# Kernel tuning notes

Measured on AMD Instinct MI355X. Metric: run time of the kernel, lower is better.

Reference implementation:

```python
import jax, jax.numpy as jnp
import numpy as np
from jax import lax

HEADS = 4
SR = 4
LN_EPS = 1e-5


def setup_inputs() -> dict:
    key = jax.random.key(0)
    ks = jax.random.split(key, 8)
    B, N, C = 8, 4096, 256
    w_scale = 0.05  # keep attention logits in a sane range
    return {
        "x": jax.random.normal(ks[0], (B, N, C), jnp.float32),
        "h": 64,
        "w": 64,
        "Wq": jax.random.normal(ks[1], (C, C), jnp.float32) * w_scale,
        "Wkv": jax.random.normal(ks[2], (C, 2 * C), jnp.float32) * w_scale,
        "sr_w": jax.random.normal(ks[3], (C, C, SR, SR), jnp.float32) * w_scale,
        "sr_b": jnp.zeros((C,), jnp.float32),
        "ln_g": jnp.ones((C,), jnp.float32),
        "ln_b": jnp.zeros((C,), jnp.float32),
        "Wo": jax.random.normal(ks[4], (C, C), jnp.float32) * w_scale,
        "bo": jnp.zeros((C,), jnp.float32),
    }


def _layernorm(x, g, b):
    mu = x.mean(-1, keepdims=True)
    var = ((x - mu) ** 2).mean(-1, keepdims=True)
    return (x - mu) * lax.rsqrt(var + LN_EPS) * g + b


def reference(x, h, w, Wq, Wkv, sr_w, sr_b, ln_g, ln_b, Wo, bo):
    B, N, C = x.shape
    hd = C // HEADS
    scale = hd ** -0.5
    # Q projection -> [B, H, N, hd]
    q = (x @ Wq).reshape(B, N, HEADS, hd).transpose(0, 2, 1, 3)
    # spatial reduction of K/V tokens: strided conv + LayerNorm
    x_kv = x.transpose(0, 2, 1).reshape(B, C, h, w)  # b (h w) c -> b c h w
    x_kv = lax.conv_general_dilated(
        x_kv, sr_w, window_strides=(SR, SR), padding="VALID",
        dimension_numbers=("NCHW", "OIHW", "NCHW"))
    x_kv = x_kv + sr_b[None, :, None, None]
    Nk = (h // SR) * (w // SR)
    x_kv = x_kv.reshape(B, C, Nk).transpose(0, 2, 1)  # b c h w -> b (h w) c
    x_kv = _layernorm(x_kv, ln_g, ln_b)
    # KV projection -> k, v each [B, H, Nk, hd]
    kv = (x_kv @ Wkv).reshape(B, Nk, 2, HEADS, hd)
    k = kv[:, :, 0].transpose(0, 2, 1, 3)
    v = kv[:, :, 1].transpose(0, 2, 1, 3)
    # attention: full [B, H, N, Nk] score matrix, softmax over kv axis
    att = jax.nn.softmax(jnp.einsum("bhxd,bhyd->bhxy", q, k) * scale, axis=-1)
    out = jnp.einsum("bhxy,bhyd->bhxd", att, v)
    out = out.transpose(0, 2, 1, 3).reshape(B, N, C)  # b h l d -> b l (h d)
    return out @ Wo + bo
```

## Files before the change

kernel.cpp:

```cpp
#include <hip/hip_runtime.h>

typedef __bf16 bf16;
typedef bf16 bf16x8 __attribute__((ext_vector_type(8)));
typedef bf16 bf16x4 __attribute__((ext_vector_type(4)));
typedef float f32x4 __attribute__((ext_vector_type(4)));

#define MFMA16(a, b, c) __builtin_amdgcn_mfma_f32_16x16x32_bf16(a, b, c, 0, 0, 0)

__device__ __forceinline__ void gload_lds16(const bf16* g, bf16* l) {
  __builtin_amdgcn_global_load_lds(
      (const __attribute__((address_space(1))) void*)g,
      (__attribute__((address_space(3))) void*)l, 16, 0, 0);
}

__global__ void k_prep(const float* __restrict__ x, const float* __restrict__ Wq,
                       const float* __restrict__ Wkv, const float* __restrict__ Wo,
                       const float* __restrict__ srw,
                       bf16* __restrict__ x_bf, bf16* __restrict__ WqT,
                       bf16* __restrict__ WkvT, bf16* __restrict__ WoT,
                       bf16* __restrict__ srwT) {
  int bid = blockIdx.x, tid = threadIdx.x;
  if (bid < 4096) {
    int i = (bid * 256 + tid) * 8;
    float4 v0 = *(const float4*)(x + i);
    float4 v1 = *(const float4*)(x + i + 4);
    bf16x8 o;
    o[0] = (bf16)v0.x; o[1] = (bf16)v0.y; o[2] = (bf16)v0.z; o[3] = (bf16)v0.w;
    o[4] = (bf16)v1.x; o[5] = (bf16)v1.y; o[6] = (bf16)v1.z; o[7] = (bf16)v1.w;
    *(bf16x8*)(x_bf + i) = o;
  } else if (bid < 5120) {
    int id = (bid - 4096) * 256 + tid;
    if (id < 65536) {
      int c = id >> 8, r = id & 255;
      WqT[c * 256 + (r ^ ((c & 7) << 3))] = (bf16)Wq[r * 256 + c];
    } else if (id < 196608) {
      int l = id - 65536;
      int c = l >> 8, r = l & 255;
      WkvT[l] = (bf16)Wkv[r * 512 + c];
    } else {
      int l = id - 196608;
      int c = l >> 8, r = l & 255;
      WoT[l] = (bf16)Wo[r * 256 + c];
    }
  } else {
    int id4 = ((bid - 5120) * 256 + tid) * 4;
    int o = id4 >> 12, rem = id4 & 4095;
    int i = rem >> 4, p = rem & 15;
    float4 v = *(const float4*)(srw + id4);
    srwT[(o << 12) + ((p + 0) << 8) + i] = (bf16)v.x;
    srwT[(o << 12) + ((p + 1) << 8) + i] = (bf16)v.y;
    srwT[(o << 12) + ((p + 2) << 8) + i] = (bf16)v.z;
    srwT[(o << 12) + ((p + 3) << 8) + i] = (bf16)v.w;
  }
}

template <int AMODE, int EMODE>
__global__ __launch_bounds__(256, 2) void k_gemm(
    const bf16* __restrict__ A, const bf16* __restrict__ Bt,
    void* __restrict__ Cout, const float* __restrict__ bias,
    int M, int N, int K) {
  constexpr int LDT = 72;
  __shared__ alignas(16) bf16 As[64 * LDT];
  __shared__ alignas(16) bf16 Bs[64 * LDT];
  int tid = threadIdx.x;
  int m0 = blockIdx.x * 64, n0 = blockIdx.y * 64;
  int kbeg = blockIdx.z * K;
  int wave = tid >> 6, lane = tid & 63;
  int quad = lane >> 4, l16 = lane & 15;

  f32x4 acc[4];
#pragma unroll
  for (int i = 0; i < 4; i++) acc[i] = (f32x4){0.f, 0.f, 0.f, 0.f};

  for (int k0 = kbeg; k0 < kbeg + K; k0 += 64) {
#pragma unroll
    for (int t = 0; t < 2; t++) {
      int c = tid + t * 256;
      int row = c >> 3, c8 = (c & 7) * 8;
      *(bf16x8*)&As[row * LDT + c8] =
          *(const bf16x8*)(A + (size_t)(m0 + row) * K + k0 + c8);
      *(bf16x8*)&Bs[row * LDT + c8] =
          *(const bf16x8*)(Bt + (size_t)(n0 + row) * K + k0 + c8);
    }
    __syncthreads();
#pragma unroll
    for (int kk = 0; kk < 64; kk += 32) {
      bf16x8 af = *(const bf16x8*)&As[(wave * 16 + l16) * LDT + kk + quad * 8];
#pragma unroll
      for (int nt = 0; nt < 4; nt++) {
        bf16x8 bfr = *(const bf16x8*)&Bs[(nt * 16 + l16) * LDT + kk + quad * 8];
        acc[nt] = MFMA16(af, bfr, acc[nt]);
      }
    }
    __syncthreads();
  }

  int rbase = m0 + wave * 16 + quad * 4;
#pragma unroll
  for (int nt = 0; nt < 4; nt++) {
    int col = n0 + nt * 16 + l16;
#pragma unroll
    for (int r = 0; r < 4; r++) {
      float v = acc[nt][r];
      int row = rbase + r;
      if constexpr (EMODE == 2) {
        int b = row >> 8, key = row & 255;
        int isv = col >> 8, c2 = col & 255;
        int hh = c2 >> 6, d = c2 & 63;
        int bh = b * 4 + hh;
        bf16* dst = (bf16*)Cout;
        if (isv == 0)
          dst[(((size_t)bh) * 256 + key) * 64 + (d ^ ((key & 7) << 3))] = (bf16)v;
        else
          dst[32 * 256 * 64 + (((size_t)bh) * 64 + d) * 256 + (key ^ ((d & 7) << 3))] = (bf16)v;
      } else {
        ((float*)Cout)[(size_t)row * N + col] = v + bias[col];
      }
    }
  }
}

template <int AMODE, int EMODE>
__global__ __launch_bounds__(256, 2) void k_gemm128(
    const bf16* __restrict__ A, const bf16* __restrict__ Bt,
    void* __restrict__ Cout, const float* __restrict__ bias,
    int M, int N, int K) {
  __shared__ alignas(16) bf16 As[128 * 64];
  __shared__ alignas(16) bf16 Bs[128 * 64];
  int tid = threadIdx.x;
  int m0 = blockIdx.x * 128, n0 = blockIdx.y * 128;
  int kbeg = blockIdx.z * K;
  int wave = tid >> 6, lane = tid & 63;
  int quad = lane >> 4, l16 = lane & 15;
  int wr = wave >> 1, wc = wave & 1;

  f32x4 acc[4][4];
#pragma unroll
  for (int i = 0; i < 4; i++)
#pragma unroll
    for (int j = 0; j < 4; j++) acc[i][j] = (f32x4){0.f, 0.f, 0.f, 0.f};

  for (int k0 = kbeg; k0 < kbeg + K; k0 += 64) {
#pragma unroll
    for (int t = 0; t < 4; t++) {
      int chunk = wave * 4 + t;
      int row = chunk * 8 + (lane >> 3);
      int c8 = (lane & 7) * 8;
      const bf16* asrc;
      if constexpr (AMODE == 0) {
        asrc = A + (size_t)(m0 + row) * K + k0 + c8;
      } else {
        int m = m0 + row;
        int b = m >> 8, tt = m & 255;
        int oh = tt >> 4, ow = tt & 15;
        int p = k0 >> 8;
        int kh = p >> 2, kw = p & 3;
        int tok = (oh * 4 + kh) * 64 + ow * 4 + kw;
        asrc = A + ((size_t)(b * 4096 + tok) << 8) + (k0 & 255) + c8;
      }
      gload_lds16(asrc, As + chunk * 512);
      gload_lds16(Bt + (size_t)(n0 + row) * ((AMODE == 1) ? 4096 : K) + k0 + c8,
                  Bs + chunk * 512);
    }
    __syncthreads();
#pragma unroll
    for (int kk = 0; kk < 64; kk += 32) {
      bf16x8 af[4], bfr[4];
#pragma unroll
      for (int mt = 0; mt < 4; mt++)
        af[mt] = *(const bf16x8*)&As[(wr * 64 + mt * 16 + l16) * 64 + kk + quad * 8];
#pragma unroll
      for (int nt = 0; nt < 4; nt++)
        bfr[nt] = *(const bf16x8*)&Bs[(wc * 64 + nt * 16 + l16) * 64 + kk + quad * 8];
#pragma unroll
      for (int mt = 0; mt < 4; mt++)
#pragma unroll
        for (int nt = 0; nt < 4; nt++)
          acc[mt][nt] = MFMA16(af[mt], bfr[nt], acc[mt][nt]);
    }
    __syncthreads();
  }

#pragma unroll
  for (int mt = 0; mt < 4; mt++) {
    int rbase = m0 + wr * 64 + mt * 16 + quad * 4;
#pragma unroll
    for (int nt = 0; nt < 4; nt++) {
      int col = n0 + wc * 64 + nt * 16 + l16;
#pragma unroll
      for (int r = 0; r < 4; r++) {
        float v = acc[mt][nt][r];
        int row = rbase + r;
        if constexpr (EMODE == 3) {
          ((float*)Cout)[(size_t)row * N + col] = v + bias[col];
        } else {
          ((float*)Cout)[((size_t)blockIdx.z * M + row) * N + col] = v;
        }
      }
    }
  }
}

__global__ __launch_bounds__(256, 3) void k_gemm_out(
    const bf16* __restrict__ A, const bf16* __restrict__ Bt,
    float* __restrict__ out, const float* __restrict__ bias) {
  __shared__ alignas(16) bf16 As[64 * 64];
  __shared__ alignas(16) bf16 Bs[256 * 64];
  int tid = threadIdx.x;
  int m0 = blockIdx.x * 64;
  int wave = tid >> 6, lane = tid & 63;
  int quad = lane >> 4, l16 = lane & 15;

  f32x4 acc[4][4];
#pragma unroll
  for (int i = 0; i < 4; i++)
#pragma unroll
    for (int j = 0; j < 4; j++) acc[i][j] = (f32x4){0.f, 0.f, 0.f, 0.f};

  for (int k0 = 0; k0 < 256; k0 += 64) {
    int c8 = (lane & 7) * 8;
#pragma unroll
    for (int t = 0; t < 2; t++) {
      int chunk = wave * 2 + t;
      int row = chunk * 8 + (lane >> 3);
      gload_lds16(A + (size_t)(m0 + row) * 256 + k0 + c8, As + chunk * 512);
    }
#pragma unroll
    for (int t = 0; t < 8; t++) {
      int chunk = wave * 8 + t;
      int row = chunk * 8 + (lane >> 3);
      gload_lds16(Bt + (size_t)row * 256 + k0 + c8, Bs + chunk * 512);
    }
    __syncthreads();
#pragma unroll
    for (int kk = 0; kk < 64; kk += 32) {
      bf16x8 af[4], bfr[4];
#pragma unroll
      for (int mt = 0; mt < 4; mt++)
        af[mt] = *(const bf16x8*)&As[(mt * 16 + l16) * 64 + kk + quad * 8];
#pragma unroll
      for (int nt = 0; nt < 4; nt++)
        bfr[nt] = *(const bf16x8*)&Bs[(wave * 64 + nt * 16 + l16) * 64 + kk + quad * 8];
#pragma unroll
      for (int mt = 0; mt < 4; mt++)
#pragma unroll
        for (int nt = 0; nt < 4; nt++)
          acc[mt][nt] = MFMA16(af[mt], bfr[nt], acc[mt][nt]);
    }
    __syncthreads();
  }

#pragma unroll
  for (int mt = 0; mt < 4; mt++) {
    int rbase = m0 + mt * 16 + quad * 4;
#pragma unroll
    for (int nt = 0; nt < 4; nt++) {
      int col = wave * 64 + nt * 16 + l16;
      float bb = bias[col];
#pragma unroll
      for (int r = 0; r < 4; r++)
        out[(size_t)(rbase + r) * 256 + col] = acc[mt][nt][r] + bb;
    }
  }
}

__global__ void k_ln(const float* __restrict__ part, const float* __restrict__ srb,
                     const float* __restrict__ g, const float* __restrict__ bb,
                     bf16* __restrict__ out) {
  int row = blockIdx.x * 4 + (threadIdx.x >> 6);
  int lane = threadIdx.x & 63;
  size_t off = (size_t)row * 256 + lane * 4;
  float4 v = *(const float4*)&part[off];
#pragma unroll
  for (int z = 1; z < 8; z++) {
    float4 p = *(const float4*)&part[(size_t)z * 2048 * 256 + off];
    v.x += p.x; v.y += p.y; v.z += p.z; v.w += p.w;
  }
  int c = lane * 4;
  v.x += srb[c + 0]; v.y += srb[c + 1]; v.z += srb[c + 2]; v.w += srb[c + 3];
  float s = v.x + v.y + v.z + v.w;
#pragma unroll
  for (int i = 1; i < 64; i <<= 1) s += __shfl_xor(s, i, 64);
  float mu = s * (1.f / 256.f);
  float d0 = v.x - mu, d1 = v.y - mu, d2 = v.z - mu, d3 = v.w - mu;
  float q = d0 * d0 + d1 * d1 + d2 * d2 + d3 * d3;
#pragma unroll
  for (int i = 1; i < 64; i <<= 1) q += __shfl_xor(q, i, 64);
  float rs = rsqrtf(q * (1.f / 256.f) + 1e-5f);
  bf16x4 o;
  o[0] = (bf16)(d0 * rs * g[c + 0] + bb[c + 0]);
  o[1] = (bf16)(d1 * rs * g[c + 1] + bb[c + 1]);
  o[2] = (bf16)(d2 * rs * g[c + 2] + bb[c + 2]);
  o[3] = (bf16)(d3 * rs * g[c + 3] + bb[c + 3]);
  *(bf16x4*)&out[(size_t)row * 256 + c] = o;
}

__global__ __launch_bounds__(256, 3) void k_attn(
    const bf16* __restrict__ xbf,
    const bf16* __restrict__ WqT,
    const bf16* __restrict__ Kg,
    const bf16* __restrict__ Vg,
    bf16* __restrict__ O) {
  int bh = blockIdx.x, qt = blockIdx.y;
  int b = bh >> 2, h = bh & 3;
  int tid = threadIdx.x, wave = tid >> 6, lane = tid & 63;
  int quad = lane >> 4, l16 = lane & 15;

  __shared__ alignas(16) bf16 smem[24576];
  bf16* R0  = smem;
  bf16* R2a = smem + 16384;
  bf16* R2b = smem + 20480;

  const bf16* Kbh = Kg + ((size_t)bh << 14);
  const bf16* Vbh = Vg + ((size_t)bh << 14);
  const bf16* Wqh = WqT + ((size_t)(h * 64) << 8);

#pragma unroll
  for (int t = 0; t < 8; t++) {
    int chunk = t * 4 + wave;
    gload_lds16(Wqh + chunk * 512 + lane * 8, R0 + chunk * 512);
  }
#pragma unroll
  for (int t = 0; t < 2; t++) {
    int chunk = wave * 2 + t;
    gload_lds16(Vbh + (chunk * 8 + (lane >> 3)) * 256 + 0 + (lane & 7) * 8,
                R2a + chunk * 512);
  }
  const bf16* xrow =
      xbf + (((size_t)(b * 4096 + qt * 64 + wave * 16 + l16)) << 8) + quad * 8;
  bf16x8 ax[8];
#pragma unroll
  for (int j = 0; j < 8; j++) ax[j] = *(const bf16x8*)(xrow + j * 32);

  __syncthreads();

  f32x4 q[4];
#pragma unroll
  for (int i = 0; i < 4; i++) q[i] = (f32x4){0.f, 0.f, 0.f, 0.f};
  __builtin_amdgcn_s_setprio(1);
#pragma unroll
  for (int j = 0; j < 8; j++) {
#pragma unroll
    for (int nt = 0; nt < 4; nt++) {
      int wrow = nt * 16 + l16;
      bf16x8 bw = *(const bf16x8*)&R0[wrow * 256 +
                                      ((j * 32 + quad * 8) ^ ((wrow & 7) << 3))];
      q[nt] = MFMA16(ax[j], bw, q[nt]);
    }
  }
  __builtin_amdgcn_s_setprio(0);
  __syncthreads();

#pragma unroll
  for (int nt = 0; nt < 4; nt++)
#pragma unroll
    for (int r = 0; r < 4; r++) {
      int qr = wave * 16 + quad * 4 + r;
      R2b[qr * 64 + ((nt * 16 + l16) ^ ((qr & 7) << 3))] = (bf16)q[nt][r];
    }
#pragma unroll
  for (int t = 0; t < 8; t++) {
    int chunk = t * 4 + wave;
    gload_lds16(Kbh + chunk * 512 + lane * 8, R0 + chunk * 512);
  }
  __syncthreads();

  int arow = wave * 16 + l16;
  int asw = (arow & 7) << 3;
  bf16x8 aq0 = *(const bf16x8*)&R2b[arow * 64 + ((quad * 8) ^ asw)];
  bf16x8 aq1 = *(const bf16x8*)&R2b[arow * 64 + ((32 + quad * 8) ^ asw)];
  asm volatile("s_waitcnt lgkmcnt(0)" ::: "memory");
#pragma unroll
  for (int t = 0; t < 2; t++) {
    int chunk = wave * 2 + t;
    gload_lds16(Vbh + (chunk * 8 + (lane >> 3)) * 256 + 64 + (lane & 7) * 8,
                R2b + chunk * 512);
  }

  f32x4 s[16];
#pragma unroll
  for (int i = 0; i < 16; i++) s[i] = (f32x4){0.f, 0.f, 0.f, 0.f};
  __builtin_amdgcn_s_setprio(1);
#pragma unroll
  for (int nt = 0; nt < 16; nt++) {
    int krow = nt * 16 + l16;
    const bf16* kb = R0 + krow * 64;
    int sw = (krow & 7) << 3;
    bf16x8 b0 = *(const bf16x8*)(kb + ((quad * 8) ^ sw));
    bf16x8 b1 = *(const bf16x8*)(kb + ((32 + quad * 8) ^ sw));
    s[nt] = MFMA16(aq0, b0, s[nt]);
    s[nt] = MFMA16(aq1, b1, s[nt]);
  }
  __builtin_amdgcn_s_setprio(0);

  const float scale = 0.125f;
#pragma unroll
  for (int r = 0; r < 4; r++) {
    float m = -1e30f;
#pragma unroll
    for (int nt = 0; nt < 16; nt++) m = fmaxf(m, s[nt][r]);
#pragma unroll
    for (int i = 1; i < 16; i <<= 1) m = fmaxf(m, __shfl_xor(m, i, 64));
    float sum = 0.f;
#pragma unroll
    for (int nt = 0; nt < 16; nt++) {
      float e = __expf((s[nt][r] - m) * scale);
      s[nt][r] = e;
      sum += e;
    }
#pragma unroll
    for (int i = 1; i < 16; i <<= 1) sum += __shfl_xor(sum, i, 64);
    float inv = 1.f / sum;
#pragma unroll
    for (int nt = 0; nt < 16; nt++) s[nt][r] *= inv;
  }

  __syncthreads();

#pragma unroll
  for (int nt = 0; nt < 16; nt++)
#pragma unroll
    for (int r = 0; r < 4; r++) {
      int prow = wave * 16 + quad * 4 + r;
      R0[prow * 256 + ((nt * 16 + l16) ^ ((prow & 7) << 3))] = (bf16)s[nt][r];
    }

  const bf16* pb = R0 + arow * 256;
  f32x4 o[4];
#pragma unroll
  for (int i = 0; i < 4; i++) o[i] = (f32x4){0.f, 0.f, 0.f, 0.f};

#pragma unroll
  for (int cq = 0; cq < 4; cq++) {
    const bf16* Vbuf = (cq & 1) ? R2b : R2a;
    __builtin_amdgcn_s_setprio(1);
#pragma unroll
    for (int k0 = 0; k0 < 64; k0 += 32) {
      bf16x8 ap = *(const bf16x8*)(pb + ((cq * 64 + k0 + quad * 8) ^ asw));
#pragma unroll
      for (int nt = 0; nt < 4; nt++) {
        int vrow = nt * 16 + l16;
        bf16x8 bv = *(const bf16x8*)&Vbuf[vrow * 64 +
                                          ((k0 + quad * 8) ^ ((vrow & 7) << 3))];
        o[nt] = MFMA16(ap, bv, o[nt]);
      }
    }
    __builtin_amdgcn_s_setprio(0);
    if (cq < 3) {
      __syncthreads();
      if (cq < 2) {
        bf16* nb = (cq & 1) ? R2b : R2a;
#pragma unroll
        for (int t = 0; t < 2; t++) {
          int chunk = wave * 2 + t;
          gload_lds16(Vbh + (chunk * 8 + (lane >> 3)) * 256 + (cq + 2) * 64 +
                          (lane & 7) * 8,
                      nb + chunk * 512);
        }
      }
    }
  }

  size_t orow = (size_t)b * 4096 + qt * 64 + wave * 16 + quad * 4;
#pragma unroll
  for (int nt = 0; nt < 4; nt++) {
    int col = h * 64 + nt * 16 + l16;
#pragma unroll
    for (int r = 0; r < 4; r++) O[(orow + r) * 256 + col] = (bf16)o[nt][r];
  }
}

extern "C" void kernel_launch(void* const* d_in, const int* in_sizes, int n_in,
                              void* d_out, int out_size, void* d_ws, size_t ws_size,
                              hipStream_t stream) {
  (void)in_sizes; (void)n_in; (void)out_size; (void)ws_size;
  const float* x   = (const float*)d_in[0];
  const float* Wq  = (const float*)d_in[3];
  const float* Wkv = (const float*)d_in[4];
  const float* srw = (const float*)d_in[5];
  const float* srb = (const float*)d_in[6];
  const float* lng = (const float*)d_in[7];
  const float* lnb = (const float*)d_in[8];
  const float* Wo  = (const float*)d_in[9];
  const float* bo  = (const float*)d_in[10];
  float* out = (float*)d_out;

  char* ws = (char*)d_ws;
  bf16*  x_bf  = (bf16*)(ws + 0);
  bf16*  AObuf = (bf16*)(ws + 16777216);
  float* convp = (float*)(ws + 33554432);
  bf16*  WqT   = (bf16*)(ws + 50331648);
  bf16*  WkvT  = (bf16*)(ws + 50462720);
  bf16*  WoT   = (bf16*)(ws + 50724864);
  bf16*  srwT  = (bf16*)(ws + 50855936);
  bf16*  xln   = (bf16*)(ws + 52953088);
  bf16*  kvbuf = (bf16*)(ws + 54001664);

  k_prep<<<6144, 256, 0, stream>>>(x, Wq, Wkv, Wo, srw, x_bf, WqT, WkvT, WoT, srwT);
  k_gemm128<1, 4><<<dim3(16, 2, 8), 256, 0, stream>>>(x_bf, srwT, convp, nullptr, 2048, 256, 512);
  k_ln<<<512, 256, 0, stream>>>(convp, srb, lng, lnb, xln);
  k_gemm<0, 2><<<dim3(32, 8), 256, 0, stream>>>(xln, WkvT, kvbuf, nullptr, 2048, 512, 256);
  k_attn<<<dim3(32, 64), 256, 0, stream>>>(x_bf, WqT, kvbuf, kvbuf + (size_t)32 * 256 * 64, AObuf);
  k_gemm_out<<<512, 256, 0, stream>>>(AObuf, WoT, out, bo);
}
```

Baseline: 176.1 us.

## Shrink attention LDS by streaming V in 32-key chunks to raise occupancy

The attention kernel's LDS footprint drops from 48KB to 40KB by replacing two 64-key V buffers with a double-buffered pair of 32-key chunks. The swizzle of the V layout changes to match the new 32-wide rows, and one barrier is removed by reading Q fragments before the K load. The launch bound goes from 3 to 4 blocks per CU to use the freed LDS. In exchange the PV loop has 8 stages, each with its own barrier, so synchronisation overhead rises and register pressure under the tighter bound may cause spills.

```diff
diff --git a/kernel.cpp b/kernel.cpp
--- a/kernel.cpp
+++ b/kernel.cpp
@@ -112,7 +112,7 @@
         if (isv == 0)
           dst[(((size_t)bh) * 256 + key) * 64 + (d ^ ((key & 7) << 3))] = (bf16)v;
         else
-          dst[32 * 256 * 64 + (((size_t)bh) * 64 + d) * 256 + (key ^ ((d & 7) << 3))] = (bf16)v;
+          dst[32 * 256 * 64 + (((size_t)bh) * 64 + d) * 256 + (key ^ ((d & 3) << 3))] = (bf16)v;
       } else {
         ((float*)Cout)[(size_t)row * N + col] = v + bias[col];
       }
@@ -295,7 +295,7 @@
   *(bf16x4*)&out[(size_t)row * 256 + c] = o;
 }
 
-__global__ __launch_bounds__(256, 3) void k_attn(
+__global__ __launch_bounds__(256, 4) void k_attn(
     const bf16* __restrict__ xbf,
     const bf16* __restrict__ WqT,
     const bf16* __restrict__ Kg,
@@ -306,10 +306,9 @@
   int tid = threadIdx.x, wave = tid >> 6, lane = tid & 63;
   int quad = lane >> 4, l16 = lane & 15;
 
-  __shared__ alignas(16) bf16 smem[24576];
-  bf16* R0  = smem;
-  bf16* R2a = smem + 16384;
-  bf16* R2b = smem + 20480;
+  __shared__ alignas(16) bf16 smem[20480];
+  bf16* R0 = smem;
+  bf16* Vq = smem + 16384;
 
   const bf16* Kbh = Kg + ((size_t)bh << 14);
   const bf16* Vbh = Vg + ((size_t)bh << 14);
@@ -319,12 +318,6 @@
   for (int t = 0; t < 8; t++) {
     int chunk = t * 4 + wave;
     gload_lds16(Wqh + chunk * 512 + lane * 8, R0 + chunk * 512);
-  }
-#pragma unroll
-  for (int t = 0; t < 2; t++) {
-    int chunk = wave * 2 + t;
-    gload_lds16(Vbh + (chunk * 8 + (lane >> 3)) * 256 + 0 + (lane & 7) * 8,
-                R2a + chunk * 512);
   }
   const bf16* xrow =
       xbf + (((size_t)(b * 4096 + qt * 64 + wave * 16 + l16)) << 8) + quad * 8;
@@ -349,33 +342,31 @@
     }
   }
   __builtin_amdgcn_s_setprio(0);
-  __syncthreads();
 
 #pragma unroll
   for (int nt = 0; nt < 4; nt++)
 #pragma unroll
     for (int r = 0; r < 4; r++) {
       int qr = wave * 16 + quad * 4 + r;
-      R2b[qr * 64 + ((nt * 16 + l16) ^ ((qr & 7) << 3))] = (bf16)q[nt][r];
-    }
+      Vq[qr * 64 + ((nt * 16 + l16) ^ ((qr & 7) << 3))] = (bf16)q[nt][r];
+    }
+  int arow = wave * 16 + l16;
+  int asw = (arow & 7) << 3;
+  bf16x8 aq0 = *(const bf16x8*)&Vq[arow * 64 + ((quad * 8) ^ asw)];
+  bf16x8 aq1 = *(const bf16x8*)&Vq[arow * 64 + ((32 + quad * 8) ^ asw)];
+  __syncthreads();
+
 #pragma unroll
   for (int t = 0; t < 8; t++) {
     int chunk = t * 4 + wave;
     gload_lds16(Kbh + chunk * 512 + lane * 8, R0 + chunk * 512);
   }
+#pragma unroll
+  for (int e = 0; e < 2; e++) {
+    gload_lds16(Vbh + (wave * 16 + (lane >> 2)) * 256 + e * 32 + (lane & 3) * 8,
+                Vq + e * 2048 + wave * 512);
+  }
   __syncthreads();
-
-  int arow = wave * 16 + l16;
-  int asw = (arow & 7) << 3;
-  bf16x8 aq0 = *(const bf16x8*)&R2b[arow * 64 + ((quad * 8) ^ asw)];
-  bf16x8 aq1 = *(const bf16x8*)&R2b[arow * 64 + ((32 + quad * 8) ^ asw)];
-  asm volatile("s_waitcnt lgkmcnt(0)" ::: "memory");
-#pragma unroll
-  for (int t = 0; t < 2; t++) {
-    int chunk = wave * 2 + t;
-    gload_lds16(Vbh + (chunk * 8 + (lane >> 3)) * 256 + 64 + (lane & 7) * 8,
-                R2b + chunk * 512);
-  }
 
   f32x4 s[16];
 #pragma unroll
@@ -431,32 +422,24 @@
   for (int i = 0; i < 4; i++) o[i] = (f32x4){0.f, 0.f, 0.f, 0.f};
 
 #pragma unroll
-  for (int cq = 0; cq < 4; cq++) {
-    const bf16* Vbuf = (cq & 1) ? R2b : R2a;
+  for (int e = 0; e < 8; e++) {
+    const bf16* Vbuf = Vq + (e & 1) * 2048;
     __builtin_amdgcn_s_setprio(1);
-#pragma unroll
-    for (int k0 = 0; k0 < 64; k0 += 32) {
-      bf16x8 ap = *(const bf16x8*)(pb + ((cq * 64 + k0 + quad * 8) ^ asw));
-#pragma unroll
-      for (int nt = 0; nt < 4; nt++) {
-        int vrow = nt * 16 + l16;
-        bf16x8 bv = *(const bf16x8*)&Vbuf[vrow * 64 +
-                                          ((k0 + quad * 8) ^ ((vrow & 7) << 3))];
-        o[nt] = MFMA16(ap, bv, o[nt]);
-      }
+    bf16x8 ap = *(const bf16x8*)(pb + ((e * 32 + quad * 8) ^ asw));
+#pragma unroll
+    for (int nt = 0; nt < 4; nt++) {
+      int vrow = nt * 16 + l16;
+      bf16x8 bv = *(const bf16x8*)&Vbuf[vrow * 32 +
+                                        ((quad * 8) ^ ((vrow & 3) << 3))];
+      o[nt] = MFMA16(ap, bv, o[nt]);
     }
     __builtin_amdgcn_s_setprio(0);
-    if (cq < 3) {
+    if (e < 7) {
       __syncthreads();
-      if (cq < 2) {
-        bf16* nb = (cq & 1) ? R2b : R2a;
-#pragma unroll
-        for (int t = 0; t < 2; t++) {
-          int chunk = wave * 2 + t;
-          gload_lds16(Vbh + (chunk * 8 + (lane >> 3)) * 256 + (cq + 2) * 64 +
-                          (lane & 7) * 8,
-                      nb + chunk * 512);
-        }
+      if (e < 6) {
+        gload_lds16(
+            Vbh + (wave * 16 + (lane >> 2)) * 256 + (e + 2) * 32 + (lane & 3) * 8,
+            Vq + (e & 1) * 2048 + wave * 512);
       }
     }
   }
```

After: 172.7 us. Within noise of the previous version (-2.0%).
